# Kernel optimization log

Measured on AMD Instinct MI355X. Metric: run time of the kernel, lower is better.

Reference implementation:

```python
import jax, jax.numpy as jnp
import numpy as np

TEMPERATURE = 1.0  # anneal_state_params['tempature'] at init
EPS_ZERO = 1e-5
EPS_DIV = 1e-29

N, M, K, D = 200000, 64, 16, 32

def setup_inputs() -> dict:
    key = jax.random.key(0)
    k1, k2, k3 = jax.random.split(key, 3)
    T = jax.random.normal(k1, (N, D), dtype=jnp.float32)
    alpha = jax.random.uniform(k2, (M, K, D), dtype=jnp.float32)  # np.random.rand init
    th = jnp.zeros((M, K), dtype=jnp.float32)
    # ambiguity thresholds: column 0 = pos (>0), column 1 = neg (<0)
    a = jax.random.uniform(k3, (M, K, 2), dtype=jnp.float32) * 0.5 + 0.1
    amb = a * jnp.array([1.0, -1.0], dtype=jnp.float32)
    return {"T": T, "alpha": alpha, "th": th, "amb": amb}

def reference(T, alpha, th, amb):
    # per-fern softmax over the feature axis of alpha*temperature
    sa = jax.nn.softmax(alpha * TEMPERATURE, axis=-1)          # (M, K, D)
    # batched fern projections: one einsum replaces the per-fern matmul loop
    temp = jnp.einsum('nd,mkd->nmk', T, sa)                    # (N, M, K)
    temp = jnp.where(jnp.abs(temp) < EPS_ZERO, 0.0, temp)
    b = temp - th[None, :, :]                                  # subtract threshold
    pos = amb[None, :, :, 0]                                   # (1, M, K)
    neg = amb[None, :, :, 1]
    B = jnp.clip((b - neg) / (pos - neg + EPS_DIV), 0.0, 1.0)  # (N, M, K)
    return B
```

## Files before the change

kernel.cpp:

```cpp
#include <hip/hip_runtime.h>
#include <math.h>

#define N_TOT 200000
#define D_    32
#define MK    1024
#define EPS_DIV  1e-29f

#define ROWS  16
#define COLS  128
#define NT    8
#define NMKE  (MK / COLS)
#define NTILE (N_TOT / ROWS)
#define NBLK  4096
#define WQ    ((NBLK * 4) / NMKE)
#define LDSW  132

typedef __attribute__((ext_vector_type(8))) short short8;
typedef __attribute__((ext_vector_type(4))) float f32x4;

__device__ __forceinline__ unsigned short f2bf(float x) {
    unsigned int u = __float_as_uint(x);
    u += 0x7FFFu + ((u >> 16) & 1u);
    return (unsigned short)(u >> 16);
}
__device__ __forceinline__ float bf2f(unsigned short h) {
    return __uint_as_float(((unsigned int)h) << 16);
}

__global__ __launch_bounds__(256) void prep_kernel(
    const float* __restrict__ alpha, const float* __restrict__ th,
    const float* __restrict__ amb,
    unsigned short* __restrict__ Whi, unsigned short* __restrict__ Wlo,
    float* __restrict__ off)
{
    int mk = blockIdx.x * 256 + threadIdx.x;
    if (mk >= MK) return;
    float v[D_];
    float mx = -1e30f;
#pragma unroll
    for (int d = 0; d < D_; ++d) { v[d] = alpha[mk * D_ + d]; mx = fmaxf(mx, v[d]); }
    float sum = 0.f;
#pragma unroll
    for (int d = 0; d < D_; ++d) { v[d] = expf(v[d] - mx); sum += v[d]; }
    float pos = amb[mk * 2 + 0];
    float neg = amb[mk * 2 + 1];
    float s  = 1.0f / (pos - neg + EPS_DIV);
    float si = s / sum;
#pragma unroll
    for (int d = 0; d < D_; ++d) {
        float w = v[d] * si;
        unsigned short h = f2bf(w);
        Whi[mk * D_ + d] = h;
        Wlo[mk * D_ + d] = f2bf(w - bf2f(h));
    }
    off[mk] = (0.0f - th[mk] - neg) * s;
}

__global__ __launch_bounds__(256, 4) void fern_mfma(
    const float* __restrict__ T,
    const unsigned short* __restrict__ Whi, const unsigned short* __restrict__ Wlo,
    const float* __restrict__ off, float* __restrict__ out)
{
    __shared__ float stage[4][ROWS][LDSW];

    const int tid     = threadIdx.x;
    const int lane    = tid & 63;
    const int wid     = tid >> 6;
    const int wave_id = blockIdx.x * 4 + wid;
    const int mke     = wave_id & (NMKE - 1);
    const int wq      = wave_id >> 3;
    const int lc      = lane & 15;
    const int lk      = lane >> 4;
    const int il      = lane & 31;
    const int mk0     = mke * COLS;

    short8 wh[NT], wl[NT];
#pragma unroll
    for (int t = 0; t < NT; ++t) {
        long c = (long)(mk0 + t * 16 + lc);
        wh[t] = *(const short8*)(Whi + c * D_ + lk * 8);
        wl[t] = *(const short8*)(Wlo + c * D_ + lk * 8);
    }
    const f32x4 ofv = *(const f32x4*)(off + mk0 + 4 * il);

    float* sw = &stage[wid][lc][0];

    for (int tile = wq; tile < NTILE; tile += WQ) {
        const int n0 = tile * ROWS;

        const float* tp = T + (long)(n0 + lc) * D_ + lk * 8;
        float4 v0 = *(const float4*)tp;
        float4 v1 = *(const float4*)(tp + 4);
        float xs[8] = { v0.x, v0.y, v0.z, v0.w, v1.x, v1.y, v1.z, v1.w };
        short8 ah, al;
#pragma unroll
        for (int j = 0; j < 8; ++j) {
            unsigned short h = f2bf(xs[j]);
            ah[j] = (short)h;
            al[j] = (short)f2bf(xs[j] - bf2f(h));
        }

#pragma unroll
        for (int t = 0; t < NT; ++t) {
            f32x4 acc = { 0.f, 0.f, 0.f, 0.f };
            acc = __builtin_amdgcn_mfma_f32_16x16x32_bf16(wh[t], ah, acc, 0, 0, 0);
            acc = __builtin_amdgcn_mfma_f32_16x16x32_bf16(wh[t], al, acc, 0, 0, 0);
            acc = __builtin_amdgcn_mfma_f32_16x16x32_bf16(wl[t], ah, acc, 0, 0, 0);
            *(f32x4*)(sw + t * 16 + lk * 4) = acc;
        }

#pragma unroll
        for (int s = 0; s < 8; ++s) {
            const int r = 2 * s + (lane >> 5);
            f32x4 v = *(const f32x4*)(&stage[wid][r][4 * il]);
            f32x4 rr;
#pragma unroll
            for (int j = 0; j < 4; ++j)
                rr[j] = fminf(fmaxf(v[j] + ofv[j], 0.f), 1.f);
            *(f32x4*)(out + (long)(n0 + r) * MK + mk0 + 4 * il) = rr;
        }
    }
}

extern "C" void kernel_launch(void* const* d_in, const int* in_sizes, int n_in,
                              void* d_out, int out_size, void* d_ws, size_t ws_size,
                              hipStream_t stream)
{
    const float* T     = (const float*)d_in[0];
    const float* alpha = (const float*)d_in[1];
    const float* th    = (const float*)d_in[2];
    const float* amb   = (const float*)d_in[3];
    float* out = (float*)d_out;

    unsigned short* Whi = (unsigned short*)d_ws;
    unsigned short* Wlo = Whi + MK * D_;
    float* offp = (float*)(Wlo + MK * D_);

    prep_kernel<<<MK / 256, 256, 0, stream>>>(alpha, th, amb, Whi, Wlo, offp);
    fern_mfma<<<NBLK, 256, 0, stream>>>(T, Whi, Wlo, offp, out);
}
```

Before: 189.7 us.

## Share LDS staging across block and write 2KB contiguous row segments

Restructures the work split so each block owns 16 rows and half of the 1024 output columns, with the four waves each computing 128 columns into a shared XOR-swizzled LDS tile. Each output row segment written per task grows from 512B to 2KB, which is meant to improve write coalescing and DRAM efficiency on this store-bound kernel. In exchange it adds two block-wide barriers per task and a larger shared tile.

```diff
diff --git a/kernel.cpp b/kernel.cpp
--- a/kernel.cpp
+++ b/kernel.cpp
@@ -6,14 +6,13 @@
 #define MK    1024
 #define EPS_DIV  1e-29f
 
-#define ROWS  16
-#define COLS  128
-#define NT    8
-#define NMKE  (MK / COLS)
-#define NTILE (N_TOT / ROWS)
-#define NBLK  4096
-#define WQ    ((NBLK * 4) / NMKE)
-#define LDSW  132
+#define ROWS   16
+#define HALF   512
+#define NT     8
+#define NSTRIP (N_TOT / ROWS)
+#define NTASK  (NSTRIP * 2)
+#define NBLK   4096
+#define LDSF   512
 
 typedef __attribute__((ext_vector_type(8))) short short8;
 typedef __attribute__((ext_vector_type(4))) float f32x4;
@@ -61,18 +60,16 @@
     const unsigned short* __restrict__ Whi, const unsigned short* __restrict__ Wlo,
     const float* __restrict__ off, float* __restrict__ out)
 {
-    __shared__ float stage[4][ROWS][LDSW];
+    __shared__ float stage[ROWS][LDSF];
 
-    const int tid     = threadIdx.x;
-    const int lane    = tid & 63;
-    const int wid     = tid >> 6;
-    const int wave_id = blockIdx.x * 4 + wid;
-    const int mke     = wave_id & (NMKE - 1);
-    const int wq      = wave_id >> 3;
-    const int lc      = lane & 15;
-    const int lk      = lane >> 4;
-    const int il      = lane & 31;
-    const int mk0     = mke * COLS;
+    const int tid  = threadIdx.x;
+    const int lane = tid & 63;
+    const int wid  = tid >> 6;
+    const int lc   = lane & 15;
+    const int lk   = lane >> 4;
+    const int half = blockIdx.x & 1;
+    const int mkb  = half * HALF;
+    const int mk0  = mkb + wid * 128;
 
     short8 wh[NT], wl[NT];
 #pragma unroll
@@ -81,12 +78,12 @@
         wh[t] = *(const short8*)(Whi + c * D_ + lk * 8);
         wl[t] = *(const short8*)(Wlo + c * D_ + lk * 8);
     }
-    const f32x4 ofv = *(const f32x4*)(off + mk0 + 4 * il);
+    const int sc  = tid & 127;
+    const int sr0 = tid >> 7;
+    const f32x4 ofv = *(const f32x4*)(off + mkb + 4 * sc);
 
-    float* sw = &stage[wid][lc][0];
-
-    for (int tile = wq; tile < NTILE; tile += WQ) {
-        const int n0 = tile * ROWS;
+    for (int task = blockIdx.x; task < NTASK; task += NBLK) {
+        const int n0 = (task >> 1) * ROWS;
 
         const float* tp = T + (long)(n0 + lc) * D_ + lk * 8;
         float4 v0 = *(const float4*)tp;
@@ -106,19 +103,23 @@
             acc = __builtin_amdgcn_mfma_f32_16x16x32_bf16(wh[t], ah, acc, 0, 0, 0);
             acc = __builtin_amdgcn_mfma_f32_16x16x32_bf16(wh[t], al, acc, 0, 0, 0);
             acc = __builtin_amdgcn_mfma_f32_16x16x32_bf16(wl[t], ah, acc, 0, 0, 0);
-            *(f32x4*)(sw + t * 16 + lk * 4) = acc;
+            const int chunk = (wid * 32 + t * 4 + lk) ^ (lc & 7);
+            *(f32x4*)&stage[lc][chunk * 4] = acc;
         }
+        __syncthreads();
 
 #pragma unroll
         for (int s = 0; s < 8; ++s) {
-            const int r = 2 * s + (lane >> 5);
-            f32x4 v = *(const f32x4*)(&stage[wid][r][4 * il]);
+            const int r = 2 * s + sr0;
+            const int k = sc ^ (r & 7);
+            f32x4 v = *(const f32x4*)&stage[r][k * 4];
             f32x4 rr;
 #pragma unroll
             for (int j = 0; j < 4; ++j)
                 rr[j] = fminf(fmaxf(v[j] + ofv[j], 0.f), 1.f);
-            *(f32x4*)(out + (long)(n0 + r) * MK + mk0 + 4 * il) = rr;
+            *(f32x4*)(out + (long)(n0 + r) * MK + mkb + 4 * sc) = rr;
         }
+        __syncthreads();
     }
 }
 
```

Result: faster. 168.0 us (median of 2 runs) (-11.4%).
